# Optimization experiments

Measured on AMD Instinct MI355X. Metric: run time of the kernel, lower is better.

The kernel has to match this reference:

```python
import jax, jax.numpy as jnp
import numpy as np

KSIZE = 3
KN = (KSIZE - 1) // 2  # 1
TEMP = 50.0


def _extract_patches(x, same_pad):
    """TF tf.image.extract_patches ordering: per location, (dy, dx, channel).
    x: [b,H,W,d] -> [b,h,w,9*d] (h=H,w=W if same_pad else H-2,W-2)."""
    if same_pad:
        x = jnp.pad(x, ((0, 0), (KN, KN), (KN, KN), (0, 0)))
    b, Hp, Wp, d = x.shape
    h, w = Hp - 2 * KN, Wp - 2 * KN
    slices = [x[:, dy:dy + h, dx:dx + w, :]
              for dy in range(KSIZE) for dx in range(KSIZE)]
    return jnp.concatenate(slices, axis=-1)


def setup_inputs() -> dict:
    key = jax.random.key(0)
    k1, k2, k3 = jax.random.split(key, 3)
    b, h, w, dims = 4, 48, 48, 64
    g_in = jax.random.normal(k1, (b, h, w, dims), dtype=jnp.float32)
    # binary inpainting mask (1 = known background, 0 = hole)
    mask = (jax.random.uniform(k2, (b, h, w, 1)) > 0.5).astype(jnp.float32)
    W2 = jax.random.normal(k3, (2 * dims, dims), dtype=jnp.float32) / np.sqrt(2.0 * dims)
    b2 = jnp.zeros((dims,), dtype=jnp.float32)
    return {"g_in": g_in, "mask": mask, "W2": W2, "b2": b2}


def reference(g_in, mask, W2, b2):
    b, h, w, dims = g_in.shape
    c = (h - 2 * KN) * (w - 2 * KN)

    mask_r = mask  # already (h,w,1); broadcasts over dims (== tile)
    bg = g_in * mask_r

    # p1: VALID 3x3 patches of bg -> dynamic kernels, [b, c, 9*dims]
    p1 = _extract_patches(bg, same_pad=False).reshape(b, c, KSIZE * KSIZE * dims)
    # p2: SAME 3x3 patches of g_in, [b, h, w, 9*dims]
    p2 = _extract_patches(g_in, same_pad=True)

    # cross-correlation: conv2d(ft, k1) == per-location dot with each bg patch
    CS = jnp.einsum('byxk,bjk->byxj', p2, p1)              # [b,h,w,c]
    k1d = jnp.sum(p1 * p1, axis=2)                          # [b,c]
    wwd = jnp.sum(p2 * p2, axis=3, keepdims=True)           # [b,h,w,1]
    DS1 = k1d[:, None, None, :] + wwd - 2.0 * CS            # squared distances
    mu = jnp.mean(DS1, axis=3, keepdims=True)
    sd = jnp.std(DS1, axis=3, keepdims=True)                # population std (tf.math.reduce_std)
    DS2 = -jnp.tanh((DS1 - mu) / sd)
    CA = jax.nn.softmax(TEMP * DS2, axis=-1)                # [b,h,w,c]

    # transposed conv aggregation with per-sample kernels k2[b,j,dy,dx,ch]
    k2 = p1.reshape(b, c, KSIZE, KSIZE, dims)
    CA_pad = jnp.pad(CA, ((0, 0), (KN, KN), (KN, KN), (0, 0)))
    acl = jnp.zeros((b, h, w, dims), dtype=g_in.dtype)
    for dy in range(KSIZE):
        for dx in range(KSIZE):
            win = CA_pad[:, 2 * KN - dy:2 * KN - dy + h, 2 * KN - dx:2 * KN - dx + w, :]
            acl = acl + jnp.einsum('byxj,bjd->byxd', win, k2[:, :, dy, dx, :])
    acl = acl / 9.0

    ACL = bg + acl * (1.0 - mask_r)
    con1 = jnp.concatenate([g_in, ACL], axis=3)             # [b,h,w,2*dims]
    return jax.nn.elu(jnp.einsum('byxk,kd->byxd', con1, W2) + b2)
```

## Files before the change

kernel.cpp:

```cpp
#include <hip/hip_runtime.h>
#include <hip/hip_fp16.h>
#include <math.h>

#define BB 4
#define HH 48
#define WW 48
#define DD 64
#define CH 46
#define CWp 46
#define CC (CH*CWp)
#define KK 576
#define HWp (HH*WW)
#define KPAD 2176
#define KSPLIT0 1088
#define PW 50
#define PP (PW*PW)

typedef __attribute__((ext_vector_type(8))) short short8;
typedef __attribute__((ext_vector_type(4))) float float4v;

#define OFFB_GPAD  ((size_t)0)
#define OFFB_BGPAD ((size_t)1280000)
#define OFFB_E     ((size_t)2560000)
#define OFFB_K1D   ((size_t)2596864)
#define OFFB_P1T   ((size_t)2630720)
#define OFFB_S     ((size_t)12657728)
#define OFFB_AGG0  ((size_t)52765760)
#define OFFB_AGG1  ((size_t)63382592)

__device__ __forceinline__ ushort f2bf(float x) {
    unsigned u = __float_as_uint(x);
    return (ushort)((u + 0x7FFFu + ((u >> 16) & 1u)) >> 16);
}

__device__ __forceinline__ float waveReduceSum(float x) {
#pragma unroll
    for (int o = 32; o > 0; o >>= 1) x += __shfl_down(x, o, 64);
    return x;
}

__device__ __forceinline__ float blockReduceSum(float x, float* sm) {
#pragma unroll
    for (int o = 32; o > 0; o >>= 1) x += __shfl_down(x, o, 64);
    int lane = threadIdx.x & 63, w = threadIdx.x >> 6;
    __syncthreads();
    if (lane == 0) sm[w] = x;
    __syncthreads();
    return sm[0] + sm[1] + sm[2] + sm[3];
}

__device__ __forceinline__ float fast_tanh(float z) {
    float e = __expf(2.f * z);
    return 1.f - 2.f / (e + 1.f);
}

typedef __attribute__((address_space(3))) void lds_void_t;
typedef __attribute__((address_space(1))) void gmem_void_t;
__device__ __forceinline__ void gld16(const ushort* g, ushort* lds) {
    __builtin_amdgcn_global_load_lds((gmem_void_t*)g, (lds_void_t*)lds, 16, 0, 0);
}

__global__ __launch_bounds__(256) void build_pads(const float* __restrict__ g,
                                                  const float* __restrict__ mask,
                                                  ushort* __restrict__ gpad,
                                                  ushort* __restrict__ bgpad,
                                                  float* __restrict__ e) {
    int w = threadIdx.x >> 6, c = threadIdx.x & 63;
    int q4 = blockIdx.x * 4 + w;
    int b = q4 / PP, q = q4 % PP;
    int yp = q / PW, xp = q % PW;
    size_t o = (size_t)q4 * DD + c;
    if (yp >= 1 && yp <= HH && xp >= 1 && xp <= WW) {
        int pix = (yp - 1) * WW + (xp - 1);
        float gv = g[((size_t)b * HWp + pix) * DD + c];
        float m  = mask[(size_t)b * HWp + pix];
        float bgv = gv * m;
        gpad[o]  = f2bf(gv);
        bgpad[o] = f2bf(bgv);
        float ss = waveReduceSum(bgv * bgv);
        if (c == 0) e[b * HWp + pix] = ss;
    } else {
        gpad[o] = 0;
        bgpad[o] = 0;
    }
}

__global__ __launch_bounds__(256) void build_p1t(const ushort* __restrict__ bgpad,
                                                 const float* __restrict__ e,
                                                 ushort* __restrict__ p1t,
                                                 float* __restrict__ k1d) {
    int d9 = blockIdx.y, b = blockIdx.z;
    int t = threadIdx.x;
    if (blockIdx.x == 34) {
        int jg = (b * 9 + d9) * 256 + t;
        if (jg < BB * CC) {
            int bb = jg / CC, j = jg % CC;
            int jy = j / CWp, jx = j - jy * CWp;
            const float* eb = e + bb * HWp + jy * WW + jx;
            float s = 0.f;
#pragma unroll
            for (int ddy = 0; ddy < 3; ddy++)
#pragma unroll
                for (int ddx = 0; ddx < 3; ddx++) s += eb[ddy * WW + ddx];
            k1d[jg] = s;
        }
        return;
    }
    __shared__ ushort T[64 * 65];
    int jt = blockIdx.x;
    int dy = d9 / 3, dx = d9 - dy * 3;
    const ushort* src = bgpad + (size_t)b * PP * DD;
    int lr = t >> 3, c8 = (t & 7) * 8;
#pragma unroll
    for (int pass = 0; pass < 2; pass++) {
        int r = lr + pass * 32;
        int j = jt * 64 + r;
        uint4 d = make_uint4(0, 0, 0, 0);
        if (j < CC) {
            int jy = j / CWp, jx = j - jy * CWp;
            d = *(const uint4*)(src + (size_t)((jy + dy + 1) * PW + (jx + dx + 1)) * DD + c8);
        }
        ushort tmp[8];
        *(uint4*)tmp = d;
#pragma unroll
        for (int u = 0; u < 8; u++) T[r * 65 + c8 + u] = tmp[u];
    }
    __syncthreads();
#pragma unroll
    for (int pass = 0; pass < 2; pass++) {
        int c = lr + pass * 32;
        int j8 = (t & 7) * 8;
        ushort tmp[8];
#pragma unroll
        for (int u = 0; u < 8; u++) tmp[u] = T[(j8 + u) * 65 + c];
        *(uint4*)(p1t + ((size_t)b * KK + d9 * 64 + c) * KPAD + jt * 64 + j8) = *(const uint4*)tmp;
    }
}

__global__ __launch_bounds__(256) void gemm1_nt(const ushort* __restrict__ gpad,
                                                const ushort* __restrict__ bgpad,
                                                __half* __restrict__ Cout) {
    __shared__ ushort As[2 * 4096];
    __shared__ ushort Bs[2 * 4096];
    int i0 = blockIdx.x;
    int b = (i0 & 7) >> 1;
    int tile = ((i0 >> 3) << 1) | (i0 & 1);
    int ty = tile / 17, tx = tile - ty * 17;
    int m0 = ty * 128, n0 = tx * 128;
    const ushort* Ag = gpad + (size_t)b * PP * DD;
    const ushort* Bg = bgpad + (size_t)b * PP * DD;

    int tid = threadIdx.x;
    int l = tid & 63, w = tid >> 6;
    int quad = l >> 4, l15 = l & 15;
    int sw8 = (l15 >> 1) & 3;
    int wm = (w >> 1) * 64, wn = (w & 1) * 64;
    int rowInC = l >> 2;
    int cSw = (l & 3) ^ ((l >> 3) & 3);

    int baseA[2], baseB[2];
    bool vB[2];
#pragma unroll
    for (int i = 0; i < 2; i++) {
        int rg = w * 2 + i;
        int r = rg * 16 + rowInC;
        int p = m0 + r;
        int y = p / WW, x = p - y * WW;
        baseA[i] = (y * PW + x) * DD + cSw * 8;
        int n = n0 + r;
        vB[i] = (n < CC);
        int jy = 0, jx = 0;
        if (vB[i]) { jy = n / CWp; jx = n - jy * CWp; }
        baseB[i] = ((jy + 1) * PW + (jx + 1)) * DD + cSw * 8;
    }

    float4v acc[4][4];
#pragma unroll
    for (int i = 0; i < 4; i++)
#pragma unroll
        for (int j = 0; j < 4; j++) acc[i][j] = (float4v){0.f, 0.f, 0.f, 0.f};

#pragma unroll
    for (int i = 0; i < 2; i++) {
        int rg = w * 2 + i;
        gld16(Ag + baseA[i], As + rg * 512);
        if (vB[i]) gld16(Bg + baseB[i], Bs + rg * 512);
    }

    int buf = 0;
    for (int k0 = 0; k0 < KK; k0 += 32) {
        __syncthreads();
        int nb = buf ^ 1;
        int kn = k0 + 32;
        if (kn < KK) {
            int d9 = kn >> 6;
            int dy = d9 / 3, dx = d9 - dy * 3;
            int off = (dy * PW + dx) * DD + (kn & 63);
#pragma unroll
            for (int i = 0; i < 2; i++) {
                int rg = w * 2 + i;
                gld16(Ag + baseA[i] + off, As + nb * 4096 + rg * 512);
                if (vB[i]) gld16(Bg + baseB[i] + off, Bs + nb * 4096 + rg * 512);
            }
        }
        const ushort* Ax = As + buf * 4096;
        const ushort* Bx = Bs + buf * 4096;
        short8 af[4], bf[4];
#pragma unroll
        for (int i = 0; i < 4; i++)
            af[i] = *(const short8*)&Ax[(wm + i * 16 + l15) * 32 + ((quad ^ sw8)) * 8];
#pragma unroll
        for (int j = 0; j < 4; j++)
            bf[j] = *(const short8*)&Bx[(wn + j * 16 + l15) * 32 + ((quad ^ sw8)) * 8];
#pragma unroll
        for (int i = 0; i < 4; i++)
#pragma unroll
            for (int j = 0; j < 4; j++)
                acc[i][j] = __builtin_amdgcn_mfma_f32_16x16x32_bf16(af[i], bf[j], acc[i][j], 0, 0, 0);
        buf = nb;
    }

    __half* C = Cout + (size_t)b * HWp * KPAD;
#pragma unroll
    for (int i = 0; i < 4; i++) {
#pragma unroll
        for (int j = 0; j < 4; j++) {
            int n = n0 + wn + j * 16 + l15;
            if (n < CC) {
#pragma unroll
                for (int r = 0; r < 4; r++) {
                    int m = m0 + wm + i * 16 + quad * 4 + r;
                    C[(size_t)m * KPAD + n] = __float2half(acc[i][j][r]);
                }
            }
        }
    }
}

template <int NF, bool NMASK>
__device__ __forceinline__ void gemm_tile_db(const ushort* __restrict__ Ab,
                                             const ushort* __restrict__ Bb,
                                             int lda, int ldb, int kb, int ke,
                                             int Nrem,
                                             ushort* As, ushort* Bs,
                                             float4v (&acc)[4][NF]) {
    constexpr int NBI = NF / 2;
    constexpr int BBUF = 2048 * NBI;
    int tid = threadIdx.x;
    int l = tid & 63, w = tid >> 6;
    int quad = l >> 4, l15 = l & 15;
    int sw8 = (l15 >> 1) & 3;
    int wm = (w >> 1) * 64, wn = (w & 1) * (NF * 16);
    int rowInC = l >> 2;
    int cSw = (l & 3) ^ ((l >> 3) & 3);

#pragma unroll
    for (int i = 0; i < 2; i++) {
        int rg = w * 2 + i;
        gld16(Ab + (size_t)(rg * 16 + rowInC) * lda + kb + cSw * 8, As + rg * 512);
    }
#pragma unroll
    for (int i = 0; i < NBI; i++) {
        int rg = w * NBI + i;
        int r = rg * 16 + rowInC;
        if (!NMASK || r < Nrem)
            gld16(Bb + (size_t)r * ldb + kb + cSw * 8, Bs + rg * 512);
    }

    int buf = 0;
    for (int k0 = kb; k0 < ke; k0 += 32) {
        __syncthreads();
        int nb = buf ^ 1;
        if (k0 + 32 < ke) {
#pragma unroll
            for (int i = 0; i < 2; i++) {
                int rg = w * 2 + i;
                gld16(Ab + (size_t)(rg * 16 + rowInC) * lda + (k0 + 32) + cSw * 8,
                      As + nb * 4096 + rg * 512);
            }
#pragma unroll
            for (int i = 0; i < NBI; i++) {
                int rg = w * NBI + i;
                int r = rg * 16 + rowInC;
                if (!NMASK || r < Nrem)
                    gld16(Bb + (size_t)r * ldb + (k0 + 32) + cSw * 8,
                          Bs + nb * BBUF + rg * 512);
            }
        }
        const ushort* Ax = As + buf * 4096;
        const ushort* Bx = Bs + buf * BBUF;
        short8 af[4], bf[NF];
#pragma unroll
        for (int i = 0; i < 4; i++)
            af[i] = *(const short8*)&Ax[(wm + i * 16 + l15) * 32 + ((quad ^ sw8)) * 8];
#pragma unroll
        for (int j = 0; j < NF; j++)
            bf[j] = *(const short8*)&Bx[(wn + j * 16 + l15) * 32 + ((quad ^ sw8)) * 8];
#pragma unroll
        for (int i = 0; i < 4; i++)
#pragma unroll
            for (int j = 0; j < NF; j++)
                acc[i][j] = __builtin_amdgcn_mfma_f32_16x16x32_bf16(af[i], bf[j], acc[i][j], 0, 0, 0);
        buf = nb;
    }
}

__global__ __launch_bounds__(256) void gemm2_split(const ushort* __restrict__ A,
                                                   const ushort* __restrict__ Bt,
                                                   __half* __restrict__ agg0,
                                                   __half* __restrict__ agg1) {
    __shared__ ushort As[2 * 4096];
    __shared__ ushort Bs[2 * 6144];
    int i0 = blockIdx.x;
    int z = i0 & 7;
    int b = z >> 1, split = z & 1;
    int tile = i0 >> 3;
    int ty = tile / 3, tx = tile - ty * 3;
    int m0 = ty * 128, n0 = tx * 192;
    const ushort* Ab = A + (size_t)b * HWp * KPAD + (size_t)m0 * KPAD;
    const ushort* Bb = Bt + (size_t)b * KK * KPAD + (size_t)n0 * KPAD;
    float4v acc[4][6];
#pragma unroll
    for (int i = 0; i < 4; i++)
#pragma unroll
        for (int j = 0; j < 6; j++) acc[i][j] = (float4v){0.f, 0.f, 0.f, 0.f};

    gemm_tile_db<6, false>(Ab, Bb, KPAD, KPAD, split ? KSPLIT0 : 0,
                           split ? KPAD : KSPLIT0, 192, As, Bs, acc);

    int tid = threadIdx.x;
    int lane = tid & 63, wid = tid >> 6;
    int quad = lane >> 4, l15 = lane & 15;
    int wm = (wid >> 1) * 64, wn = (wid & 1) * 96;
    __half* C = (split ? agg1 : agg0) + (size_t)b * HWp * KK;
#pragma unroll
    for (int i = 0; i < 4; i++) {
#pragma unroll
        for (int j = 0; j < 6; j++) {
            int n = n0 + wn + j * 16 + l15;
#pragma unroll
            for (int r = 0; r < 4; r++) {
                int m = m0 + wm + i * 16 + quad * 4 + r;
                C[(size_t)m * KK + n] = __float2half(acc[i][j][r]);
            }
        }
    }
}

__global__ __launch_bounds__(256) void rowsoft(void* __restrict__ Sbase,
                                               const float* __restrict__ k1d) {
    __shared__ float sm[4];
    size_t row = blockIdx.x;
    int b = (int)(row / HWp);
    const __half* p = (const __half*)Sbase + row * KPAD;
    ushort* wout = (ushort*)Sbase + row * KPAD;
    const float* k1 = k1d + (size_t)b * CC;
    int t = threadIdx.x;
    bool hasx = t < 34;

    uint4 raw = *(const uint4*)(p + t * 8);
    uint rx = hasx ? *(const uint*)(p + 2048 + t * 2) : 0u;
    float v[8], vx[2];
    {
        const __half2* h2 = (const __half2*)&raw;
#pragma unroll
        for (int i = 0; i < 4; i++) {
            float2 f = __half22float2(h2[i]);
            v[2 * i] = f.x; v[2 * i + 1] = f.y;
        }
        __half2 hx = *(__half2*)&rx;
        float2 fx = __half22float2(hx);
        vx[0] = fx.x; vx[1] = fx.y;
    }
    {
        const float* kp = k1 + t * 8;
#pragma unroll
        for (int i = 0; i < 8; i++) v[i] = kp[i] - 2.f * v[i];
        if (hasx) {
            vx[0] = k1[2048 + t * 2] - 2.f * vx[0];
            vx[1] = k1[2048 + t * 2 + 1] - 2.f * vx[1];
        }
    }
    float s = 0.f;
#pragma unroll
    for (int i = 0; i < 8; i++) s += v[i];
    if (hasx) s += vx[0] + vx[1];
    s = blockReduceSum(s, sm);
    float mu = s / (float)CC;
    float vs = 0.f;
#pragma unroll
    for (int i = 0; i < 8; i++) { float d = v[i] - mu; vs += d * d; }
    if (hasx) { float d0 = vx[0] - mu, d1 = vx[1] - mu; vs += d0 * d0 + d1 * d1; }
    vs = blockReduceSum(vs, sm);
    float inv_sd = 1.f / sqrtf(vs / (float)CC);
    float es = 0.f;
#pragma unroll
    for (int i = 0; i < 8; i++) {
        v[i] = __expf(-50.f * fast_tanh((v[i] - mu) * inv_sd));
        es += v[i];
    }
    if (hasx) {
        vx[0] = __expf(-50.f * fast_tanh((vx[0] - mu) * inv_sd));
        vx[1] = __expf(-50.f * fast_tanh((vx[1] - mu) * inv_sd));
        es += vx[0] + vx[1];
    }
    es = blockReduceSum(es, sm);
    float invz = 1.f / es;

    ushort o[8];
#pragma unroll
    for (int i = 0; i < 8; i++) o[i] = f2bf(v[i] * invz);
    *(uint4*)(wout + t * 8) = *(const uint4*)o;
    if (hasx) {
        ushort ox[2] = { f2bf(vx[0] * invz), f2bf(vx[1] * invz) };
        *(uint*)(wout + 2048 + t * 2) = *(const uint*)ox;
    } else {
        *(uint*)(wout + CC + 2 * (t - 34)) = 0u;
    }
}

__global__ __launch_bounds__(256) void final_k(const float* __restrict__ g,
                                               const float* __restrict__ mask,
                                               const __half* __restrict__ agg0,
                                               const __half* __restrict__ agg1,
                                               const float* __restrict__ W2,
                                               const float* __restrict__ b2,
                                               float* __restrict__ out) {
    int w = threadIdx.x >> 6, d = threadIdx.x & 63;
    int pix = blockIdx.x * 4 + w;
    int b = pix / HWp, yx = pix % HWp;
    int y = yx / WW, x = yx % WW;

    __shared__ float con1[4][128];
    float acl = 0.f;
#pragma unroll
    for (int dy = 0; dy < 3; dy++) {
#pragma unroll
        for (int dx = 0; dx < 3; dx++) {
            int yy = y + 1 - dy, xx = x + 1 - dx;
            if (yy >= 0 && yy < HH && xx >= 0 && xx < WW) {
                size_t off = ((size_t)(b * HWp + yy * WW + xx)) * KK + (dy * 3 + dx) * DD + d;
                acl += __half2float(agg0[off]) + __half2float(agg1[off]);
            }
        }
    }
    float m = mask[pix];
    float gv = g[(size_t)pix * DD + d];
    float bgv = gv * m;
    float ACL = bgv + (acl / 9.f) * (1.f - m);
    con1[w][d] = gv;
    con1[w][64 + d] = ACL;
    __syncthreads();
    float accv = b2[d];
#pragma unroll 8
    for (int k = 0; k < 128; k++) accv = fmaf(con1[w][k], W2[k * 64 + d], accv);
    out[(size_t)pix * DD + d] = accv > 0.f ? accv : expm1f(accv);
}

extern "C" void kernel_launch(void* const* d_in, const int* in_sizes, int n_in,
                              void* d_out, int out_size, void* d_ws, size_t ws_size,
                              hipStream_t stream) {
    const float* g    = (const float*)d_in[0];
    const float* mask = (const float*)d_in[1];
    const float* W2   = (const float*)d_in[2];
    const float* b2   = (const float*)d_in[3];
    float* out = (float*)d_out;
    char* ws = (char*)d_ws;

    ushort* gpad  = (ushort*)(ws + OFFB_GPAD);
    ushort* bgpad = (ushort*)(ws + OFFB_BGPAD);
    float*  e     = (float*) (ws + OFFB_E);
    float*  k1d   = (float*) (ws + OFFB_K1D);
    ushort* p1t   = (ushort*)(ws + OFFB_P1T);
    void*   S     = (void*)  (ws + OFFB_S);
    __half* agg0  = (__half*)(ws + OFFB_AGG0);
    __half* agg1  = (__half*)(ws + OFFB_AGG1);

    build_pads<<<BB * PP / 4, 256, 0, stream>>>(g, mask, gpad, bgpad, e);
    build_p1t<<<dim3(35, 9, BB), 256, 0, stream>>>(bgpad, e, p1t, k1d);

    gemm1_nt<<<dim3(1224), 256, 0, stream>>>(gpad, bgpad, (__half*)S);

    rowsoft<<<BB * HWp, 256, 0, stream>>>(S, k1d);

    gemm2_split<<<dim3(432), 256, 0, stream>>>((const ushort*)S, p1t, agg0, agg1);

    final_k<<<BB * HWp / 4, 256, 0, stream>>>(g, mask, agg0, agg1, W2, b2, out);
}
```

Measured before the change: 188.5 us.

## Factor patch cross-correlation into pixel-level Gram GEMM plus 9-tap gather

The K=576 patch-by-patch GEMM is replaced by a K=64 pixel-by-pixel Gram matrix (Q) between padded g and bg pixels. The softmax kernel then rebuilds each patch correlation by summing 9 shifted Q entries before normalising. Columns use a 48-wide slot layout so the shifted reads stay contiguous, which changes the padding of p1t, k1d and CA. This cuts the first GEMM's FLOPs about ninefold, at the cost of a larger fp16 Q buffer (2500x2304 per batch) and nine gathered reads per output, plus extra rounding from summing fp16 partials.

```diff
diff --git a/kernel.cpp b/kernel.cpp
--- a/kernel.cpp
+++ b/kernel.cpp
@@ -11,10 +11,16 @@
 #define CC (CH*CWp)
 #define KK 576
 #define HWp (HH*WW)
-#define KPAD 2176
-#define KSPLIT0 1088
 #define PW 50
 #define PP (PW*PW)
+
+#define SLOTW 48
+#define NSLOT 2208
+#define NGRP 276
+#define KPAD NSLOT
+#define KSPLIT0 1120
+#define QW 2304
+#define QROWS 2500
 
 typedef __attribute__((ext_vector_type(8))) short short8;
 typedef __attribute__((ext_vector_type(4))) float float4v;
@@ -23,10 +29,11 @@
 #define OFFB_BGPAD ((size_t)1280000)
 #define OFFB_E     ((size_t)2560000)
 #define OFFB_K1D   ((size_t)2596864)
-#define OFFB_P1T   ((size_t)2630720)
-#define OFFB_S     ((size_t)12657728)
-#define OFFB_AGG0  ((size_t)52765760)
-#define OFFB_AGG1  ((size_t)63382592)
+#define OFFB_P1T   ((size_t)2632192)
+#define OFFB_S     ((size_t)12806656)
+#define OFFB_AGG0  ((size_t)53504512)
+#define OFFB_AGG1  ((size_t)64121344)
+#define OFFB_Q     ((size_t)74738176)
 
 __device__ __forceinline__ ushort f2bf(float x) {
     unsigned u = __float_as_uint(x);
@@ -39,14 +46,14 @@
     return x;
 }
 
-__device__ __forceinline__ float blockReduceSum(float x, float* sm) {
+__device__ __forceinline__ float blockReduce5(float x, float* sm) {
 #pragma unroll
     for (int o = 32; o > 0; o >>= 1) x += __shfl_down(x, o, 64);
     int lane = threadIdx.x & 63, w = threadIdx.x >> 6;
     __syncthreads();
     if (lane == 0) sm[w] = x;
     __syncthreads();
-    return sm[0] + sm[1] + sm[2] + sm[3];
+    return sm[0] + sm[1] + sm[2] + sm[3] + sm[4];
 }
 
 __device__ __forceinline__ float fast_tanh(float z) {
@@ -91,17 +98,19 @@
                                                  float* __restrict__ k1d) {
     int d9 = blockIdx.y, b = blockIdx.z;
     int t = threadIdx.x;
-    if (blockIdx.x == 34) {
+    if (blockIdx.x == 35) {
         int jg = (b * 9 + d9) * 256 + t;
-        if (jg < BB * CC) {
-            int bb = jg / CC, j = jg % CC;
-            int jy = j / CWp, jx = j - jy * CWp;
-            const float* eb = e + bb * HWp + jy * WW + jx;
+        if (jg < BB * NSLOT) {
+            int bb = jg / NSLOT, st = jg - bb * NSLOT;
+            int jy = st / SLOTW, jx = st - jy * SLOTW;
             float s = 0.f;
-#pragma unroll
-            for (int ddy = 0; ddy < 3; ddy++)
-#pragma unroll
-                for (int ddx = 0; ddx < 3; ddx++) s += eb[ddy * WW + ddx];
+            if (jx < CWp) {
+                const float* eb = e + bb * HWp + jy * WW + jx;
+#pragma unroll
+                for (int ddy = 0; ddy < 3; ddy++)
+#pragma unroll
+                    for (int ddx = 0; ddx < 3; ddx++) s += eb[ddy * WW + ddx];
+            }
             k1d[jg] = s;
         }
         return;
@@ -114,12 +123,11 @@
 #pragma unroll
     for (int pass = 0; pass < 2; pass++) {
         int r = lr + pass * 32;
-        int j = jt * 64 + r;
+        int st = jt * 64 + r;
+        int jy = st / SLOTW, jx = st - jy * SLOTW;
         uint4 d = make_uint4(0, 0, 0, 0);
-        if (j < CC) {
-            int jy = j / CWp, jx = j - jy * CWp;
+        if (jx < CWp && jy < CWp)
             d = *(const uint4*)(src + (size_t)((jy + dy + 1) * PW + (jx + dx + 1)) * DD + c8);
-        }
         ushort tmp[8];
         *(uint4*)tmp = d;
 #pragma unroll
@@ -130,22 +138,24 @@
     for (int pass = 0; pass < 2; pass++) {
         int c = lr + pass * 32;
         int j8 = (t & 7) * 8;
+        int col0 = jt * 64 + j8;
         ushort tmp[8];
 #pragma unroll
         for (int u = 0; u < 8; u++) tmp[u] = T[(j8 + u) * 65 + c];
-        *(uint4*)(p1t + ((size_t)b * KK + d9 * 64 + c) * KPAD + jt * 64 + j8) = *(const uint4*)tmp;
-    }
-}
-
-__global__ __launch_bounds__(256) void gemm1_nt(const ushort* __restrict__ gpad,
-                                                const ushort* __restrict__ bgpad,
-                                                __half* __restrict__ Cout) {
+        if (col0 < NSLOT)
+            *(uint4*)(p1t + ((size_t)b * KK + d9 * 64 + c) * NSLOT + col0) = *(const uint4*)tmp;
+    }
+}
+
+__global__ __launch_bounds__(256) void qgemm(const ushort* __restrict__ gpad,
+                                             const ushort* __restrict__ bgpad,
+                                             __half* __restrict__ Qout) {
     __shared__ ushort As[2 * 4096];
     __shared__ ushort Bs[2 * 4096];
     int i0 = blockIdx.x;
     int b = (i0 & 7) >> 1;
     int tile = ((i0 >> 3) << 1) | (i0 & 1);
-    int ty = tile / 17, tx = tile - ty * 17;
+    int ty = tile / 18, tx = tile - ty * 18;
     int m0 = ty * 128, n0 = tx * 128;
     const ushort* Ag = gpad + (size_t)b * PP * DD;
     const ushort* Bg = bgpad + (size_t)b * PP * DD;
@@ -158,53 +168,30 @@
     int rowInC = l >> 2;
     int cSw = (l & 3) ^ ((l >> 3) & 3);
 
-    int baseA[2], baseB[2];
-    bool vB[2];
 #pragma unroll
     for (int i = 0; i < 2; i++) {
         int rg = w * 2 + i;
         int r = rg * 16 + rowInC;
-        int p = m0 + r;
-        int y = p / WW, x = p - y * WW;
-        baseA[i] = (y * PW + x) * DD + cSw * 8;
+        int u = m0 + r; if (u > QROWS - 1) u = QROWS - 1;
         int n = n0 + r;
-        vB[i] = (n < CC);
-        int jy = 0, jx = 0;
-        if (vB[i]) { jy = n / CWp; jx = n - jy * CWp; }
-        baseB[i] = ((jy + 1) * PW + (jx + 1)) * DD + cSw * 8;
-    }
-
+        int vy = n / 48, vx = n - vy * 48;
+        int baseA = u * DD + cSw * 8;
+        int baseB = ((vy + 1) * PW + (vx + 1)) * DD + cSw * 8;
+        gld16(Ag + baseA, As + rg * 512);
+        gld16(Bg + baseB, Bs + rg * 512);
+        gld16(Ag + baseA + 32, As + 4096 + rg * 512);
+        gld16(Bg + baseB + 32, Bs + 4096 + rg * 512);
+    }
     float4v acc[4][4];
 #pragma unroll
     for (int i = 0; i < 4; i++)
 #pragma unroll
         for (int j = 0; j < 4; j++) acc[i][j] = (float4v){0.f, 0.f, 0.f, 0.f};
-
-#pragma unroll
-    for (int i = 0; i < 2; i++) {
-        int rg = w * 2 + i;
-        gld16(Ag + baseA[i], As + rg * 512);
-        if (vB[i]) gld16(Bg + baseB[i], Bs + rg * 512);
-    }
-
-    int buf = 0;
-    for (int k0 = 0; k0 < KK; k0 += 32) {
-        __syncthreads();
-        int nb = buf ^ 1;
-        int kn = k0 + 32;
-        if (kn < KK) {
-            int d9 = kn >> 6;
-            int dy = d9 / 3, dx = d9 - dy * 3;
-            int off = (dy * PW + dx) * DD + (kn & 63);
-#pragma unroll
-            for (int i = 0; i < 2; i++) {
-                int rg = w * 2 + i;
-                gld16(Ag + baseA[i] + off, As + nb * 4096 + rg * 512);
-                if (vB[i]) gld16(Bg + baseB[i] + off, Bs + nb * 4096 + rg * 512);
-            }
-        }
-        const ushort* Ax = As + buf * 4096;
-        const ushort* Bx = Bs + buf * 4096;
+    __syncthreads();
+#pragma unroll
+    for (int kb = 0; kb < 2; kb++) {
+        const ushort* Ax = As + kb * 4096;
+        const ushort* Bx = Bs + kb * 4096;
         short8 af[4], bf[4];
 #pragma unroll
         for (int i = 0; i < 4; i++)
@@ -217,23 +204,108 @@
 #pragma unroll
             for (int j = 0; j < 4; j++)
                 acc[i][j] = __builtin_amdgcn_mfma_f32_16x16x32_bf16(af[i], bf[j], acc[i][j], 0, 0, 0);
-        buf = nb;
-    }
-
-    __half* C = Cout + (size_t)b * HWp * KPAD;
+    }
+    __half* C = Qout + (size_t)b * QROWS * QW;
 #pragma unroll
     for (int i = 0; i < 4; i++) {
 #pragma unroll
         for (int j = 0; j < 4; j++) {
             int n = n0 + wn + j * 16 + l15;
-            if (n < CC) {
-#pragma unroll
-                for (int r = 0; r < 4; r++) {
-                    int m = m0 + wm + i * 16 + quad * 4 + r;
-                    C[(size_t)m * KPAD + n] = __float2half(acc[i][j][r]);
-                }
-            }
-        }
+#pragma unroll
+            for (int r = 0; r < 4; r++) {
+                int m = m0 + wm + i * 16 + quad * 4 + r;
+                if (m < QROWS) C[(size_t)m * QW + n] = __float2half(acc[i][j][r]);
+            }
+        }
+    }
+}
+
+__device__ __forceinline__ void gather9(const __half* __restrict__ qb2,
+                                        const float* __restrict__ k1,
+                                        int g, float (&ds)[8], int& slot0, int& vc) {
+    int jy = g / 6;
+    int jxb = (g - jy * 6) * 8;
+    slot0 = jy * SLOTW + jxb;
+    vc = (jxb == 40) ? 6 : 8;
+    float cs[8] = {0.f, 0.f, 0.f, 0.f, 0.f, 0.f, 0.f, 0.f};
+    constexpr int UO[9] = {0, 1, 2, 50, 51, 52, 100, 101, 102};
+    constexpr int VO[9] = {0, 1, 2, 48, 49, 50, 96, 97, 98};
+#pragma unroll
+    for (int s = 0; s < 9; s++) {
+        const __half* p = qb2 + (size_t)UO[s] * QW + slot0;
+        if ((VO[s] & 1) == 0) {
+            uint4 d = *(const uint4*)(p + VO[s]);
+            const __half2* h2 = (const __half2*)&d;
+#pragma unroll
+            for (int k = 0; k < 4; k++) {
+                float2 f = __half22float2(h2[k]);
+                cs[2 * k] += f.x; cs[2 * k + 1] += f.y;
+            }
+        } else {
+            uint4 d = *(const uint4*)(p + VO[s] - 1);
+            uint e2 = *(const uint*)(p + VO[s] + 7);
+            uint wv[5] = {d.x, d.y, d.z, d.w, e2};
+#pragma unroll
+            for (int k = 0; k < 4; k++) {
+                uint a = (wv[k] >> 16) | (wv[k + 1] << 16);
+                __half2 h2 = *(__half2*)&a;
+                float2 f = __half22float2(h2);
+                cs[2 * k] += f.x; cs[2 * k + 1] += f.y;
+            }
+        }
+    }
+    float4 ka = *(const float4*)(k1 + slot0);
+    float4 kb = *(const float4*)(k1 + slot0 + 4);
+    float kk[8] = {ka.x, ka.y, ka.z, ka.w, kb.x, kb.y, kb.z, kb.w};
+#pragma unroll
+    for (int u = 0; u < 8; u++) ds[u] = kk[u] - 2.f * cs[u];
+}
+
+__global__ __launch_bounds__(320) void qrowsoft(const __half* __restrict__ Q,
+                                                const float* __restrict__ k1d,
+                                                ushort* __restrict__ CA) {
+    __shared__ float sm[5];
+    int i0 = blockIdx.x;
+    int b = (i0 & 7) >> 1;
+    int yx = ((i0 >> 3) << 1) | (i0 & 1);
+    int y = yx / WW, x = yx - y * WW;
+    size_t row = (size_t)b * HWp + yx;
+    const __half* qb2 = Q + ((size_t)b * QROWS + y * PW + x) * QW;
+    const float* k1 = k1d + (size_t)b * NSLOT;
+    ushort* wout = CA + row * (size_t)NSLOT;
+
+    int t = threadIdx.x;
+    bool act = (t < NGRP);
+    int slot0 = 0, vc = 0;
+    float ds[8] = {0.f, 0.f, 0.f, 0.f, 0.f, 0.f, 0.f, 0.f};
+    if (act) gather9(qb2, k1, t, ds, slot0, vc);
+
+    float sum = 0.f;
+#pragma unroll
+    for (int u = 0; u < 8; u++) if (u < vc) sum += ds[u];
+    sum = blockReduce5(sum, sm);
+    float mu = sum / (float)CC;
+
+    float vs = 0.f;
+#pragma unroll
+    for (int u = 0; u < 8; u++) if (u < vc) { float d = ds[u] - mu; vs += d * d; }
+    vs = blockReduce5(vs, sm);
+    float inv_sd = 1.f / sqrtf(vs / (float)CC);
+
+    float es = 0.f;
+#pragma unroll
+    for (int u = 0; u < 8; u++) {
+        ds[u] = (u < vc) ? __expf(-50.f * fast_tanh((ds[u] - mu) * inv_sd)) : 0.f;
+        es += ds[u];
+    }
+    es = blockReduce5(es, sm);
+    float invz = 1.f / es;
+
+    if (act) {
+        ushort o[8];
+#pragma unroll
+        for (int u = 0; u < 8; u++) o[u] = f2bf(ds[u] * invz);
+        *(uint4*)(wout + slot0) = *(const uint4*)o;
     }
 }
 
@@ -347,78 +419,6 @@
     }
 }
 
-__global__ __launch_bounds__(256) void rowsoft(void* __restrict__ Sbase,
-                                               const float* __restrict__ k1d) {
-    __shared__ float sm[4];
-    size_t row = blockIdx.x;
-    int b = (int)(row / HWp);
-    const __half* p = (const __half*)Sbase + row * KPAD;
-    ushort* wout = (ushort*)Sbase + row * KPAD;
-    const float* k1 = k1d + (size_t)b * CC;
-    int t = threadIdx.x;
-    bool hasx = t < 34;
-
-    uint4 raw = *(const uint4*)(p + t * 8);
-    uint rx = hasx ? *(const uint*)(p + 2048 + t * 2) : 0u;
-    float v[8], vx[2];
-    {
-        const __half2* h2 = (const __half2*)&raw;
-#pragma unroll
-        for (int i = 0; i < 4; i++) {
-            float2 f = __half22float2(h2[i]);
-            v[2 * i] = f.x; v[2 * i + 1] = f.y;
-        }
-        __half2 hx = *(__half2*)&rx;
-        float2 fx = __half22float2(hx);
-        vx[0] = fx.x; vx[1] = fx.y;
-    }
-    {
-        const float* kp = k1 + t * 8;
-#pragma unroll
-        for (int i = 0; i < 8; i++) v[i] = kp[i] - 2.f * v[i];
-        if (hasx) {
-            vx[0] = k1[2048 + t * 2] - 2.f * vx[0];
-            vx[1] = k1[2048 + t * 2 + 1] - 2.f * vx[1];
-        }
-    }
-    float s = 0.f;
-#pragma unroll
-    for (int i = 0; i < 8; i++) s += v[i];
-    if (hasx) s += vx[0] + vx[1];
-    s = blockReduceSum(s, sm);
-    float mu = s / (float)CC;
-    float vs = 0.f;
-#pragma unroll
-    for (int i = 0; i < 8; i++) { float d = v[i] - mu; vs += d * d; }
-    if (hasx) { float d0 = vx[0] - mu, d1 = vx[1] - mu; vs += d0 * d0 + d1 * d1; }
-    vs = blockReduceSum(vs, sm);
-    float inv_sd = 1.f / sqrtf(vs / (float)CC);
-    float es = 0.f;
-#pragma unroll
-    for (int i = 0; i < 8; i++) {
-        v[i] = __expf(-50.f * fast_tanh((v[i] - mu) * inv_sd));
-        es += v[i];
-    }
-    if (hasx) {
-        vx[0] = __expf(-50.f * fast_tanh((vx[0] - mu) * inv_sd));
-        vx[1] = __expf(-50.f * fast_tanh((vx[1] - mu) * inv_sd));
-        es += vx[0] + vx[1];
-    }
-    es = blockReduceSum(es, sm);
-    float invz = 1.f / es;
-
-    ushort o[8];
-#pragma unroll
-    for (int i = 0; i < 8; i++) o[i] = f2bf(v[i] * invz);
-    *(uint4*)(wout + t * 8) = *(const uint4*)o;
-    if (hasx) {
-        ushort ox[2] = { f2bf(vx[0] * invz), f2bf(vx[1] * invz) };
-        *(uint*)(wout + 2048 + t * 2) = *(const uint*)ox;
-    } else {
-        *(uint*)(wout + CC + 2 * (t - 34)) = 0u;
-    }
-}
-
 __global__ __launch_bounds__(256) void final_k(const float* __restrict__ g,
                                                const float* __restrict__ mask,
                                                const __half* __restrict__ agg0,
@@ -472,18 +472,18 @@
     float*  e     = (float*) (ws + OFFB_E);
     float*  k1d   = (float*) (ws + OFFB_K1D);
     ushort* p1t   = (ushort*)(ws + OFFB_P1T);
-    void*   S     = (void*)  (ws + OFFB_S);
+    ushort* CA    = (ushort*)(ws + OFFB_S);
     __half* agg0  = (__half*)(ws + OFFB_AGG0);
     __half* agg1  = (__half*)(ws + OFFB_AGG1);
+    __half* Qbuf  = (__half*)(ws + OFFB_Q);
 
     build_pads<<<BB * PP / 4, 256, 0, stream>>>(g, mask, gpad, bgpad, e);
-    build_p1t<<<dim3(35, 9, BB), 256, 0, stream>>>(bgpad, e, p1t, k1d);
-
-    gemm1_nt<<<dim3(1224), 256, 0, stream>>>(gpad, bgpad, (__half*)S);
-
-    rowsoft<<<BB * HWp, 256, 0, stream>>>(S, k1d);
-
-    gemm2_split<<<dim3(432), 256, 0, stream>>>((const ushort*)S, p1t, agg0, agg1);
+    build_p1t<<<dim3(36, 9, BB), 256, 0, stream>>>(bgpad, e, p1t, k1d);
+
+    qgemm<<<1440, 256, 0, stream>>>(gpad, bgpad, Qbuf);
+    qrowsoft<<<BB * HWp, 320, 0, stream>>>(Qbuf, k1d, CA);
+
+    gemm2_split<<<432, 256, 0, stream>>>(CA, p1t, agg0, agg1);
 
     final_k<<<BB * HWp / 4, 256, 0, stream>>>(g, mask, agg0, agg1, W2, b2, out);
 }
```

Result: slower. 192.5 us (+2.1%).
